# Kernel tuning notes

Measured on AMD Instinct MI355X. Metric: run time of the kernel, lower is better.

The kernel has to match this reference:

```python
import jax, jax.numpy as jnp
import numpy as np

L, H, P, R = 4096, 1024, 512, 16
DT_MIN, DT_MAX = 1e-3, 1e-1

def setup_inputs() -> dict:
    key = jax.random.key(0)
    ks = jax.random.split(key, 16)
    return {
        "input_sequence": jax.random.normal(ks[0], (L, H), jnp.float32),
        # HiPPO-like eigenvalues: negative real part, spread imaginary part
        "Lambda_re": (-0.5 * jax.random.uniform(ks[1], (P,), jnp.float32) - 1e-2),
        "Lambda_im": 3.0 * jax.random.normal(ks[2], (P,), jnp.float32),
        "B_re": jax.random.normal(ks[3], (P, H), jnp.float32) / np.float32(np.sqrt(H)),
        "B_im": jax.random.normal(ks[4], (P, H), jnp.float32) / np.float32(np.sqrt(H)),
        "C_re": jax.random.normal(ks[5], (H, 2 * P), jnp.float32) / np.float32(np.sqrt(2 * P)),
        "C_im": jax.random.normal(ks[6], (H, 2 * P), jnp.float32) / np.float32(np.sqrt(2 * P)),
        "E_re": 0.01 * jax.random.normal(ks[7], (P, R), jnp.float32),
        "E_im": 0.01 * jax.random.normal(ks[8], (P, R), jnp.float32),
        "F_re": 0.01 * jax.random.normal(ks[9], (R, P), jnp.float32),
        "F_im": 0.01 * jax.random.normal(ks[10], (R, P), jnp.float32),
        "D": jax.random.normal(ks[11], (H,), jnp.float32),
        "log_step": np.float32(np.log(DT_MIN)) + jax.random.uniform(ks[12], (P,), jnp.float32) * np.float32(np.log(DT_MAX) - np.log(DT_MIN)),
        "Delta_t_diag": 0.01 * jax.random.normal(ks[13], (L, R), jnp.float32),
    }

def _scan_op(q_i, q_j):
    # diagonal linear recurrence combine: x_j = A_j * x_i + b_j
    A_i, b_i = q_i
    A_j, b_j = q_j
    return (A_j * A_i, A_j * b_i + b_j)

def reference(input_sequence, Lambda_re, Lambda_im, B_re, B_im, C_re, C_im,
              E_re, E_im, F_re, F_im, D, log_step, Delta_t_diag):
    # clip_eigs=True: enforce left-half-plane
    Lam = jnp.clip(Lambda_re, None, -1e-4) + 1j * Lambda_im            # (P,)
    step = jnp.exp(log_step)                                           # (P,)  step_rescale=1.0
    # zoh discretization
    Lambda_bar = jnp.exp(Lam * step)                                   # (P,)
    B_tilde = B_re + 1j * B_im                                         # (P,H)
    B_bar = ((Lambda_bar - 1.0) / Lam)[:, None] * B_tilde              # (P,H)
    # Lambda extension: diag(E @ diag(d_l) @ F)[p] = sum_r E[p,r] d_l[r] F[r,p]
    E = E_re + 1j * E_im                                               # (P,R)
    F = F_re + 1j * F_im                                               # (R,P)
    EF = E.T * F                                                       # (R,P)
    ext = Delta_t_diag.astype(EF.dtype) @ EF                           # (L,P)
    Lambda_elements = Lambda_bar[None, :] + ext                        # (L,P)
    Bu_elements = input_sequence.astype(B_bar.dtype) @ B_bar.T         # (L,P)
    _, xs_f = jax.lax.associative_scan(_scan_op, (Lambda_elements, Bu_elements))
    _, xs_b = jax.lax.associative_scan(_scan_op, (Lambda_elements, Bu_elements), reverse=True)
    xs = jnp.concatenate((xs_f, xs_b), axis=-1)                        # (L,2P) bidirectional
    C_tilde = C_re + 1j * C_im                                         # (H,2P)
    ys = 2.0 * (xs @ C_tilde.T).real                                   # conj_sym=True -> 2*Re
    return ys + D * input_sequence                                     # feedthrough
```

## Files before the change

### kernel.cpp

```cpp
#include <hip/hip_runtime.h>

#define LL 4096
#define HH 1024
#define PP 512
#define RR 16
#define CH 128
#define CL 32

typedef _Float16 f16x8 __attribute__((ext_vector_type(8)));
typedef float f32x4 __attribute__((ext_vector_type(4)));
typedef unsigned short u16;
typedef unsigned int u32;

#define MF16(a, b, c) __builtin_amdgcn_mfma_f32_16x16x32_f16(a, b, c, 0, 0, 0)

__device__ __forceinline__ u16 h16(float x) {
  _Float16 h = (_Float16)x;
  return __builtin_bit_cast(u16, h);
}
__device__ __forceinline__ float f16f(u16 v) {
  return (float)__builtin_bit_cast(_Float16, v);
}

__global__ void precompute_kernel(const float* __restrict__ Lre, const float* __restrict__ Lim,
                                  const float* __restrict__ lst,
                                  const float* __restrict__ Ere, const float* __restrict__ Eim,
                                  const float* __restrict__ Fre, const float* __restrict__ Fim,
                                  float* __restrict__ Lbr, float* __restrict__ Lbi,
                                  float* __restrict__ cfr, float* __restrict__ cfi,
                                  float* __restrict__ EFr, float* __restrict__ EFi)
{
  int p = blockIdx.x * blockDim.x + threadIdx.x;
  if (p >= PP) return;
  float lre = fminf(Lre[p], -1e-4f);
  float lim = Lim[p];
  float st  = expf(lst[p]);
  float er  = expf(lre * st);
  float s, c;
  sincosf(lim * st, &s, &c);
  float lbr = er * c, lbi = er * s;
  Lbr[p] = lbr; Lbi[p] = lbi;
  float den = lre * lre + lim * lim;
  float nr  = lbr - 1.0f;
  cfr[p] = (nr * lre + lbi * lim) / den;
  cfi[p] = (lbi * lre - nr * lim) / den;
  for (int r = 0; r < RR; ++r) {
    float e_r = Ere[p * RR + r], e_i = Eim[p * RR + r];
    float f_r = Fre[r * PP + p], f_i = Fim[r * PP + p];
    EFr[r * PP + p] = e_r * f_r - e_i * f_i;
    EFi[r * PP + p] = e_r * f_i + e_i * f_r;
  }
}

__global__ void bbar_kernel(const float* __restrict__ Bre, const float* __restrict__ Bim,
                            const float* __restrict__ cfr, const float* __restrict__ cfi,
                            u16* __restrict__ B1)
{
  int i = blockIdx.x * blockDim.x + threadIdx.x;
  int base = i * 4;
  if (base >= PP * HH) return;
  int p = base >> 10, col = base & 1023;
  float cr = cfr[p], ci = cfi[p];
  float4 br = *(const float4*)&Bre[base];
  float4 bi = *(const float4*)&Bim[base];
  ushort4 rp, ip;
  rp.x = h16(cr*br.x - ci*bi.x); ip.x = h16(cr*bi.x + ci*br.x);
  rp.y = h16(cr*br.y - ci*bi.y); ip.y = h16(cr*bi.y + ci*br.y);
  rp.z = h16(cr*br.z - ci*bi.z); ip.z = h16(cr*bi.z + ci*br.z);
  rp.w = h16(cr*br.w - ci*bi.w); ip.w = h16(cr*bi.w + ci*br.w);
  *(ushort4*)&B1[(size_t)p * 1024 + col] = rp;
  *(ushort4*)&B1[(size_t)(PP + p) * 1024 + col] = ip;
}

__global__ void prep_c_kernel(const float* __restrict__ Cre, const float* __restrict__ Cim,
                              u32* __restrict__ B2)
{
  int i = blockIdx.x * blockDim.x + threadIdx.x;
  int base = i * 4;
  float4 a = *(const float4*)&Cre[base];
  float4 b = *(const float4*)&Cim[base];
  uint4 o;
  o.x = (u32)h16(a.x) | ((u32)h16(-b.x) << 16);
  o.y = (u32)h16(a.y) | ((u32)h16(-b.y) << 16);
  o.z = (u32)h16(a.z) | ((u32)h16(-b.z) << 16);
  o.w = (u32)h16(a.w) | ((u32)h16(-b.w) << 16);
  *(uint4*)&B2[base] = o;
}

__global__ __launch_bounds__(256) void ext_kernel(
    const float* __restrict__ Dt, const float* __restrict__ EFr, const float* __restrict__ EFi,
    u32* __restrict__ LE)
{
  int gid = blockIdx.x * 256 + threadIdx.x;
  int l  = gid >> 7;
  int pq = (gid & 127) << 2;
  float4 ar = {0.f, 0.f, 0.f, 0.f};
  float4 ai = {0.f, 0.f, 0.f, 0.f};
#pragma unroll
  for (int r = 0; r < RR; ++r) {
    float d = Dt[l * RR + r];
    float4 er = *(const float4*)&EFr[r * PP + pq];
    float4 ei = *(const float4*)&EFi[r * PP + pq];
    ar.x = fmaf(d, er.x, ar.x); ar.y = fmaf(d, er.y, ar.y);
    ar.z = fmaf(d, er.z, ar.z); ar.w = fmaf(d, er.w, ar.w);
    ai.x = fmaf(d, ei.x, ai.x); ai.y = fmaf(d, ei.y, ai.y);
    ai.z = fmaf(d, ei.z, ai.z); ai.w = fmaf(d, ei.w, ai.w);
  }
  uint4 o;
  o.x = (u32)h16(ar.x) | ((u32)h16(ai.x) << 16);
  o.y = (u32)h16(ar.y) | ((u32)h16(ai.y) << 16);
  o.z = (u32)h16(ar.z) | ((u32)h16(ai.z) << 16);
  o.w = (u32)h16(ar.w) | ((u32)h16(ai.w) << 16);
  *(uint4*)&LE[(size_t)l * PP + pq] = o;
}

template<int EPI, bool ACVT>
__global__ __launch_bounds__(256) void gemm_k(
    const void* __restrict__ Asrc, const u16* __restrict__ Bsrc, int Kp,
    float* __restrict__ out, const float* __restrict__ Dv,
    const float* __restrict__ Uep)
{
  __shared__ __align__(16) uint4 lds[2 * 16 * 64];
  int bid = blockIdx.x;
  int n0 = ((bid & 7) * 2 + ((bid >> 3) & 1)) * 64;
  int m0 = (bid >> 4) * 64;
  int t = threadIdx.x, lane = t & 63, w = t >> 6;
  int wr = w >> 1, wc = w & 1;
  int rl = lane & 15, kg = lane >> 4;
  int crow = t >> 2, cch = t & 3;
  int NT = Kp / 64;

  const float* Af = (const float*)Asrc;
  const u16*   Ah = (const u16*)Asrc;

  f32x4 acc[2][2];
  acc[0][0] = acc[0][1] = acc[1][0] = acc[1][1] = (f32x4){0.f, 0.f, 0.f, 0.f};

  struct Frags { uint4 a[2]; uint4 b[2]; };
  auto LOAD = [&](int kt) -> Frags {
    Frags f;
    if constexpr (ACVT) {
      const float* p = Af + (size_t)(m0 + crow) * Kp + kt * 64 + cch * 16;
#pragma unroll
      for (int j = 0; j < 2; ++j) {
        float4 a = *(const float4*)(p + j * 8), b = *(const float4*)(p + j * 8 + 4);
        f16x8 r;
        r[0] = (_Float16)a.x; r[1] = (_Float16)a.y; r[2] = (_Float16)a.z; r[3] = (_Float16)a.w;
        r[4] = (_Float16)b.x; r[5] = (_Float16)b.y; r[6] = (_Float16)b.z; r[7] = (_Float16)b.w;
        f.a[j] = __builtin_bit_cast(uint4, r);
      }
    } else {
      const u16* p = Ah + (size_t)(m0 + crow) * Kp + kt * 64 + cch * 16;
      f.a[0] = *(const uint4*)p;
      f.a[1] = *(const uint4*)(p + 8);
    }
    const u16* q = Bsrc + (size_t)(n0 + crow) * Kp + kt * 64 + cch * 16;
    f.b[0] = *(const uint4*)q;
    f.b[1] = *(const uint4*)(q + 8);
    return f;
  };
  auto WRITE = [&](int buf, const Frags& f) {
#pragma unroll
    for (int j = 0; j < 2; ++j) {
      int kq = cch * 2 + j;
      int c = kq & 3;
      int slot = c * 16 + ((crow & 15) ^ (c * 2));
      int segA = (crow >> 4) * 2 + (kq >> 2);
      lds[buf * 1024 + segA * 64 + slot] = f.a[j];
      lds[buf * 1024 + (8 + segA) * 64 + slot] = f.b[j];
    }
  };

  Frags nxt, far;
  WRITE(0, LOAD(0));
  nxt = LOAD(1);
  __syncthreads();

  for (int kt = 0; kt < NT; ++kt) {
    int c = kt & 1;
    if (kt + 2 < NT) far = LOAD(kt + 2);
    int rslot = kg * 16 + (rl ^ (kg * 2));
    f16x8 af[2][2], bf[2][2];
#pragma unroll
    for (int m = 0; m < 2; ++m)
#pragma unroll
      for (int ks = 0; ks < 2; ++ks) {
        int segA = (wr * 2 + m) * 2 + ks;
        int segB = 8 + (wc * 2 + m) * 2 + ks;
        af[m][ks] = __builtin_bit_cast(f16x8, lds[c * 1024 + segA * 64 + rslot]);
        bf[m][ks] = __builtin_bit_cast(f16x8, lds[c * 1024 + segB * 64 + rslot]);
      }
#pragma unroll
    for (int ks = 0; ks < 2; ++ks)
#pragma unroll
      for (int m = 0; m < 2; ++m)
#pragma unroll
        for (int n = 0; n < 2; ++n)
          acc[m][n] = MF16(af[m][ks], bf[n][ks], acc[m][n]);
    if (kt + 1 < NT) WRITE(c ^ 1, nxt);
    nxt = far;
    __syncthreads();
  }

  float* Stg = (float*)lds;
#pragma unroll
  for (int m = 0; m < 2; ++m)
#pragma unroll
    for (int n = 0; n < 2; ++n)
#pragma unroll
      for (int j = 0; j < 4; ++j)
        Stg[(wr * 32 + m * 16 + kg * 4 + j) * 68 + wc * 32 + n * 16 + rl] = acc[m][n][j];
  __syncthreads();
  int col4 = (t & 15) * 4, prow = t >> 4;
#pragma unroll
  for (int i = 0; i < 4; ++i) {
    int r = prow + 16 * i;
    float4 v = *(const float4*)&Stg[r * 68 + col4];
    size_t ob = (size_t)(m0 + r) * 1024 + n0 + col4;
    if constexpr (EPI == 1) {
      float4 u4 = *(const float4*)&Uep[ob];
      float4 dv = *(const float4*)&Dv[n0 + col4];
      v.x = 2.f * v.x + dv.x * u4.x; v.y = 2.f * v.y + dv.y * u4.y;
      v.z = 2.f * v.z + dv.z * u4.z; v.w = 2.f * v.w + dv.w * u4.w;
    }
    *(float4*)&out[ob] = v;
  }
}

__global__ __launch_bounds__(256) void scan_agg_kernel(
    const float* __restrict__ Lbr, const float* __restrict__ Lbi,
    const u32* __restrict__ LE, const float* __restrict__ P,
    float* __restrict__ aggAr, float* __restrict__ aggAi,
    float* __restrict__ aggBr, float* __restrict__ aggBi)
{
  int tid = blockIdx.x * 256 + threadIdx.x;
  int p   = tid & (PP - 1);
  int c   = (tid >> 9) & (CH - 1);
  int dir = tid >> 16;
  float lbr = Lbr[p], lbi = Lbi[p];
  float Ar = 1.f, Ai = 0.f, br = 0.f, bi = 0.f;
  int base = c * CL;
#pragma unroll
  for (int g = 0; g < CL / 8; ++g) {
    float ar8[8], ai8[8], br8[8], bi8[8];
#pragma unroll
    for (int u = 0; u < 8; ++u) {
      int l = base + g * 8 + u;
      int phys = dir ? (LL - 1 - l) : l;
      u32 v = LE[(size_t)phys * PP + p];
      ar8[u] = lbr + f16f((u16)(v & 0xffff));
      ai8[u] = lbi + f16f((u16)(v >> 16));
      br8[u] = P[(size_t)phys * 1024 + p];
      bi8[u] = P[(size_t)phys * 1024 + PP + p];
    }
#pragma unroll
    for (int u = 0; u < 8; ++u) {
      float nAr = ar8[u] * Ar - ai8[u] * Ai;
      float nAi = ar8[u] * Ai + ai8[u] * Ar;
      float nbr = fmaf(ar8[u], br, fmaf(-ai8[u], bi, br8[u]));
      float nbi = fmaf(ar8[u], bi, fmaf( ai8[u], br, bi8[u]));
      Ar = nAr; Ai = nAi; br = nbr; bi = nbi;
    }
  }
  aggAr[tid] = Ar; aggAi[tid] = Ai; aggBr[tid] = br; aggBi[tid] = bi;
}

__global__ __launch_bounds__(256) void scan_carry_kernel(
    const float* __restrict__ aggAr, const float* __restrict__ aggAi,
    const float* __restrict__ aggBr, const float* __restrict__ aggBi,
    float* __restrict__ carR, float* __restrict__ carI)
{
  int tid = blockIdx.x * 256 + threadIdx.x;
  int p   = tid & (PP - 1);
  int dir = tid >> 9;
  float xr = 0.f, xi = 0.f;
  for (int c = 0; c < CH; ++c) {
    int idx = (dir * CH + c) * PP + p;
    carR[idx] = xr; carI[idx] = xi;
    float ar = aggAr[idx], ai = aggAi[idx];
    float br = aggBr[idx], bi = aggBi[idx];
    float nr = fmaf(ar, xr, fmaf(-ai, xi, br));
    float ni = fmaf(ar, xi, fmaf( ai, xr, bi));
    xr = nr; xi = ni;
  }
}

__global__ __launch_bounds__(256) void scan_apply_kernel(
    const float* __restrict__ Lbr, const float* __restrict__ Lbi,
    const u32* __restrict__ LE, const float* __restrict__ P,
    const float* __restrict__ carR, const float* __restrict__ carI,
    u32* __restrict__ A2)
{
  int tid = blockIdx.x * 256 + threadIdx.x;
  int p   = tid & (PP - 1);
  int c   = (tid >> 9) & (CH - 1);
  int dir = tid >> 16;
  float lbr = Lbr[p], lbi = Lbi[p];
  float xr = carR[tid], xi = carI[tid];
  int base = c * CL;
  int cofs = dir * PP + p;
#pragma unroll
  for (int g = 0; g < CL / 8; ++g) {
    float ar8[8], ai8[8], br8[8], bi8[8];
#pragma unroll
    for (int u = 0; u < 8; ++u) {
      int l = base + g * 8 + u;
      int phys = dir ? (LL - 1 - l) : l;
      u32 v = LE[(size_t)phys * PP + p];
      ar8[u] = lbr + f16f((u16)(v & 0xffff));
      ai8[u] = lbi + f16f((u16)(v >> 16));
      br8[u] = P[(size_t)phys * 1024 + p];
      bi8[u] = P[(size_t)phys * 1024 + PP + p];
    }
#pragma unroll
    for (int u = 0; u < 8; ++u) {
      float nr = fmaf(ar8[u], xr, fmaf(-ai8[u], xi, br8[u]));
      float ni = fmaf(ar8[u], xi, fmaf( ai8[u], xr, bi8[u]));
      xr = nr; xi = ni;
      int l = base + g * 8 + u;
      int phys = dir ? (LL - 1 - l) : l;
      A2[(size_t)phys * 1024 + cofs] = (u32)h16(xr) | ((u32)h16(xi) << 16);
    }
  }
}

extern "C" void kernel_launch(void* const* d_in, const int* in_sizes, int n_in,
                              void* d_out, int out_size, void* d_ws, size_t ws_size,
                              hipStream_t stream)
{
  const float* U   = (const float*)d_in[0];
  const float* Lre = (const float*)d_in[1];
  const float* Lim = (const float*)d_in[2];
  const float* Bre = (const float*)d_in[3];
  const float* Bim = (const float*)d_in[4];
  const float* Cre = (const float*)d_in[5];
  const float* Cim = (const float*)d_in[6];
  const float* Ere = (const float*)d_in[7];
  const float* Eim = (const float*)d_in[8];
  const float* Fre = (const float*)d_in[9];
  const float* Fim = (const float*)d_in[10];
  const float* Dv  = (const float*)d_in[11];
  const float* lst = (const float*)d_in[12];
  const float* Dt  = (const float*)d_in[13];
  float* Y = (float*)d_out;

  char* wsb = (char*)d_ws;
  size_t o = 0;
  auto alloc = [&](size_t bytes) -> char* {
    char* r = wsb + o; o += (bytes + 255) & ~(size_t)255; return r;
  };
  float* Lbr = (float*)alloc(PP * 4);
  float* Lbi = (float*)alloc(PP * 4);
  float* cfr = (float*)alloc(PP * 4);
  float* cfi = (float*)alloc(PP * 4);
  float* EFr = (float*)alloc((size_t)RR * PP * 4);
  float* EFi = (float*)alloc((size_t)RR * PP * 4);
  u16* B1 = (u16*)alloc((size_t)1024 * 1024 * 2);
  u32* B2 = (u32*)alloc((size_t)1024 * 1024 * 4);
  u32* LE = (u32*)alloc((size_t)LL * PP * 4);
  float* P = (float*)alloc((size_t)LL * 1024 * 4);
  u32* A2 = (u32*)alloc((size_t)LL * 1024 * 4);
  const int NAGG = 2 * CH * PP;
  float* aggAr = (float*)alloc((size_t)NAGG * 4);
  float* aggAi = (float*)alloc((size_t)NAGG * 4);
  float* aggBr = (float*)alloc((size_t)NAGG * 4);
  float* aggBi = (float*)alloc((size_t)NAGG * 4);
  float* carR  = (float*)alloc((size_t)NAGG * 4);
  float* carI  = (float*)alloc((size_t)NAGG * 4);

  precompute_kernel<<<2, 256, 0, stream>>>(Lre, Lim, lst, Ere, Eim, Fre, Fim,
                                           Lbr, Lbi, cfr, cfi, EFr, EFi);
  bbar_kernel<<<PP * HH / 4 / 256, 256, 0, stream>>>(Bre, Bim, cfr, cfi, B1);
  prep_c_kernel<<<1024 * 1024 / 4 / 256, 256, 0, stream>>>(Cre, Cim, B2);
  ext_kernel<<<LL * PP / 4 / 256, 256, 0, stream>>>(Dt, EFr, EFi, LE);
  gemm_k<0, true><<<1024, 256, 0, stream>>>(U, B1, 1024, P, nullptr, nullptr);
  scan_agg_kernel<<<2 * CH * PP / 256, 256, 0, stream>>>(Lbr, Lbi, LE, P,
                                                         aggAr, aggAi, aggBr, aggBi);
  scan_carry_kernel<<<4, 256, 0, stream>>>(aggAr, aggAi, aggBr, aggBi, carR, carI);
  scan_apply_kernel<<<2 * CH * PP / 256, 256, 0, stream>>>(Lbr, Lbi, LE, P, carR, carI, A2);
  gemm_k<1, false><<<1024, 256, 0, stream>>>(A2, (const u16*)B2, 2048, Y, Dv, U);
}
```

Baseline: 123.9 us.

## Use direct global-to-LDS loads and 64x128 tiles in GEMMs, pre-convert input to fp16

The GEMM kernel now loads tiles straight from global memory into LDS with global_load_lds instead of staging them through registers, and widens each block's tile from 64x64 to 64x128, so the grid shrinks from 1024 to 512 blocks. The in-GEMM fp32-to-fp16 conversion of the input sequence is dropped; a separate kernel now converts it to fp16 beforehand. The aim is lower register pressure and fewer load instructions, plus more reuse per A tile. The cost is an extra kernel launch and extra memory traffic for the fp16 copy, and the pipeline now issues the next tile only one step ahead.

```diff
diff --git a/kernel.cpp b/kernel.cpp
--- a/kernel.cpp
+++ b/kernel.cpp
@@ -20,6 +20,11 @@
 }
 __device__ __forceinline__ float f16f(u16 v) {
   return (float)__builtin_bit_cast(_Float16, v);
+}
+__device__ __forceinline__ void gld16(const void* g, void* l) {
+  __builtin_amdgcn_global_load_lds(
+      (__attribute__((address_space(1))) void*)g,
+      (__attribute__((address_space(3))) void*)l, 16, 0, 0);
 }
 
 __global__ void precompute_kernel(const float* __restrict__ Lre, const float* __restrict__ Lim,
@@ -87,6 +92,18 @@
   *(uint4*)&B2[base] = o;
 }
 
+__global__ __launch_bounds__(256) void uconv_kernel(const float* __restrict__ U,
+                                                    u16* __restrict__ Uh)
+{
+  int i = (blockIdx.x * 256 + threadIdx.x) * 8;
+  float4 a = *(const float4*)&U[i];
+  float4 b = *(const float4*)&U[i + 4];
+  f16x8 r;
+  r[0] = (_Float16)a.x; r[1] = (_Float16)a.y; r[2] = (_Float16)a.z; r[3] = (_Float16)a.w;
+  r[4] = (_Float16)b.x; r[5] = (_Float16)b.y; r[6] = (_Float16)b.z; r[7] = (_Float16)b.w;
+  *(uint4*)&Uh[i] = __builtin_bit_cast(uint4, r);
+}
+
 __global__ __launch_bounds__(256) void ext_kernel(
     const float* __restrict__ Dt, const float* __restrict__ EFr, const float* __restrict__ EFi,
     u32* __restrict__ LE)
@@ -114,91 +131,73 @@
   *(uint4*)&LE[(size_t)l * PP + pq] = o;
 }
 
-template<int EPI, bool ACVT>
+template<int EPI>
 __global__ __launch_bounds__(256) void gemm_k(
-    const void* __restrict__ Asrc, const u16* __restrict__ Bsrc, int Kp,
+    const u16* __restrict__ Asrc, const u16* __restrict__ Bsrc, int Kp,
     float* __restrict__ out, const float* __restrict__ Dv,
     const float* __restrict__ Uep)
 {
-  __shared__ __align__(16) uint4 lds[2 * 16 * 64];
+  __shared__ __align__(16) uint4 lds[2 * 24 * 64];
   int bid = blockIdx.x;
-  int n0 = ((bid & 7) * 2 + ((bid >> 3) & 1)) * 64;
-  int m0 = (bid >> 4) * 64;
+  int n0 = (bid & 7) * 128;
+  int m0 = (bid >> 3) * 64;
   int t = threadIdx.x, lane = t & 63, w = t >> 6;
   int wr = w >> 1, wc = w & 1;
   int rl = lane & 15, kg = lane >> 4;
-  int crow = t >> 2, cch = t & 3;
   int NT = Kp / 64;
 
-  const float* Af = (const float*)Asrc;
-  const u16*   Ah = (const u16*)Asrc;
-
-  f32x4 acc[2][2];
-  acc[0][0] = acc[0][1] = acc[1][0] = acc[1][1] = (f32x4){0.f, 0.f, 0.f, 0.f};
-
-  struct Frags { uint4 a[2]; uint4 b[2]; };
-  auto LOAD = [&](int kt) -> Frags {
-    Frags f;
-    if constexpr (ACVT) {
-      const float* p = Af + (size_t)(m0 + crow) * Kp + kt * 64 + cch * 16;
-#pragma unroll
-      for (int j = 0; j < 2; ++j) {
-        float4 a = *(const float4*)(p + j * 8), b = *(const float4*)(p + j * 8 + 4);
-        f16x8 r;
-        r[0] = (_Float16)a.x; r[1] = (_Float16)a.y; r[2] = (_Float16)a.z; r[3] = (_Float16)a.w;
-        r[4] = (_Float16)b.x; r[5] = (_Float16)b.y; r[6] = (_Float16)b.z; r[7] = (_Float16)b.w;
-        f.a[j] = __builtin_bit_cast(uint4, r);
-      }
-    } else {
-      const u16* p = Ah + (size_t)(m0 + crow) * Kp + kt * 64 + cch * 16;
-      f.a[0] = *(const uint4*)p;
-      f.a[1] = *(const uint4*)(p + 8);
-    }
-    const u16* q = Bsrc + (size_t)(n0 + crow) * Kp + kt * 64 + cch * 16;
-    f.b[0] = *(const uint4*)q;
-    f.b[1] = *(const uint4*)(q + 8);
-    return f;
+  int rowx = rl ^ (2 * kg);
+  const u16* segsrc[6];
+#pragma unroll
+  for (int i = 0; i < 6; ++i) {
+    int s = w * 6 + i;
+    int isB = (s >= 8);
+    int sl = isB ? (s - 8) : s;
+    int row = (sl >> 1) * 16 + rowx;
+    int kq = (sl & 1) * 4 + kg;
+    segsrc[i] = (isB ? (Bsrc + (size_t)(n0 + row) * Kp)
+                     : (Asrc + (size_t)(m0 + row) * Kp)) + kq * 8;
+  }
+
+  f32x4 acc[2][4];
+#pragma unroll
+  for (int m = 0; m < 2; ++m)
+#pragma unroll
+    for (int n = 0; n < 4; ++n) acc[m][n] = (f32x4){0.f, 0.f, 0.f, 0.f};
+
+  auto ISSUE = [&](int kt, int buf) {
+#pragma unroll
+    for (int i = 0; i < 6; ++i)
+      gld16(segsrc[i] + kt * 64, &lds[(buf * 24 + w * 6 + i) * 64]);
   };
-  auto WRITE = [&](int buf, const Frags& f) {
-#pragma unroll
-    for (int j = 0; j < 2; ++j) {
-      int kq = cch * 2 + j;
-      int c = kq & 3;
-      int slot = c * 16 + ((crow & 15) ^ (c * 2));
-      int segA = (crow >> 4) * 2 + (kq >> 2);
-      lds[buf * 1024 + segA * 64 + slot] = f.a[j];
-      lds[buf * 1024 + (8 + segA) * 64 + slot] = f.b[j];
-    }
-  };
-
-  Frags nxt, far;
-  WRITE(0, LOAD(0));
-  nxt = LOAD(1);
+
+  ISSUE(0, 0);
   __syncthreads();
 
   for (int kt = 0; kt < NT; ++kt) {
     int c = kt & 1;
-    if (kt + 2 < NT) far = LOAD(kt + 2);
+    if (kt + 1 < NT) ISSUE(kt + 1, c ^ 1);
     int rslot = kg * 16 + (rl ^ (kg * 2));
-    f16x8 af[2][2], bf[2][2];
+    f16x8 af[2][2], bf[4][2];
 #pragma unroll
     for (int m = 0; m < 2; ++m)
 #pragma unroll
-      for (int ks = 0; ks < 2; ++ks) {
-        int segA = (wr * 2 + m) * 2 + ks;
-        int segB = 8 + (wc * 2 + m) * 2 + ks;
-        af[m][ks] = __builtin_bit_cast(f16x8, lds[c * 1024 + segA * 64 + rslot]);
-        bf[m][ks] = __builtin_bit_cast(f16x8, lds[c * 1024 + segB * 64 + rslot]);
-      }
+      for (int ks = 0; ks < 2; ++ks)
+        af[m][ks] = __builtin_bit_cast(f16x8,
+            lds[(c * 24 + (wr * 2 + m) * 2 + ks) * 64 + rslot]);
+#pragma unroll
+    for (int n = 0; n < 4; ++n)
+#pragma unroll
+      for (int ks = 0; ks < 2; ++ks)
+        bf[n][ks] = __builtin_bit_cast(f16x8,
+            lds[(c * 24 + 8 + (wc * 4 + n) * 2 + ks) * 64 + rslot]);
 #pragma unroll
     for (int ks = 0; ks < 2; ++ks)
 #pragma unroll
       for (int m = 0; m < 2; ++m)
 #pragma unroll
-        for (int n = 0; n < 2; ++n)
+        for (int n = 0; n < 4; ++n)
           acc[m][n] = MF16(af[m][ks], bf[n][ks], acc[m][n]);
-    if (kt + 1 < NT) WRITE(c ^ 1, nxt);
-    nxt = far;
     __syncthreads();
   }
 
@@ -206,16 +205,16 @@
 #pragma unroll
   for (int m = 0; m < 2; ++m)
 #pragma unroll
-    for (int n = 0; n < 2; ++n)
+    for (int n = 0; n < 4; ++n)
 #pragma unroll
       for (int j = 0; j < 4; ++j)
-        Stg[(wr * 32 + m * 16 + kg * 4 + j) * 68 + wc * 32 + n * 16 + rl] = acc[m][n][j];
+        Stg[(wr * 32 + m * 16 + kg * 4 + j) * 132 + wc * 64 + n * 16 + rl] = acc[m][n][j];
   __syncthreads();
-  int col4 = (t & 15) * 4, prow = t >> 4;
-#pragma unroll
-  for (int i = 0; i < 4; ++i) {
-    int r = prow + 16 * i;
-    float4 v = *(const float4*)&Stg[r * 68 + col4];
+  int col4 = (t & 31) * 4, prow = t >> 5;
+#pragma unroll
+  for (int i = 0; i < 8; ++i) {
+    int r = prow + 8 * i;
+    float4 v = *(const float4*)&Stg[r * 132 + col4];
     size_t ob = (size_t)(m0 + r) * 1024 + n0 + col4;
     if constexpr (EPI == 1) {
       float4 u4 = *(const float4*)&Uep[ob];
@@ -357,6 +356,7 @@
   float* EFi = (float*)alloc((size_t)RR * PP * 4);
   u16* B1 = (u16*)alloc((size_t)1024 * 1024 * 2);
   u32* B2 = (u32*)alloc((size_t)1024 * 1024 * 4);
+  u16* Uh = (u16*)alloc((size_t)LL * HH * 2);
   u32* LE = (u32*)alloc((size_t)LL * PP * 4);
   float* P = (float*)alloc((size_t)LL * 1024 * 4);
   u32* A2 = (u32*)alloc((size_t)LL * 1024 * 4);
@@ -372,11 +372,12 @@
                                            Lbr, Lbi, cfr, cfi, EFr, EFi);
   bbar_kernel<<<PP * HH / 4 / 256, 256, 0, stream>>>(Bre, Bim, cfr, cfi, B1);
   prep_c_kernel<<<1024 * 1024 / 4 / 256, 256, 0, stream>>>(Cre, Cim, B2);
+  uconv_kernel<<<LL * HH / 8 / 256, 256, 0, stream>>>(U, Uh);
   ext_kernel<<<LL * PP / 4 / 256, 256, 0, stream>>>(Dt, EFr, EFi, LE);
-  gemm_k<0, true><<<1024, 256, 0, stream>>>(U, B1, 1024, P, nullptr, nullptr);
+  gemm_k<0><<<512, 256, 0, stream>>>(Uh, B1, 1024, P, nullptr, nullptr);
   scan_agg_kernel<<<2 * CH * PP / 256, 256, 0, stream>>>(Lbr, Lbi, LE, P,
                                                          aggAr, aggAi, aggBr, aggBi);
   scan_carry_kernel<<<4, 256, 0, stream>>>(aggAr, aggAi, aggBr, aggBi, carR, carI);
   scan_apply_kernel<<<2 * CH * PP / 256, 256, 0, stream>>>(Lbr, Lbi, LE, P, carR, carI, A2);
-  gemm_k<1, false><<<1024, 256, 0, stream>>>(A2, (const u16*)B2, 2048, Y, Dv, U);
-}
+  gemm_k<1><<<512, 256, 0, stream>>>((const u16*)A2, (const u16*)B2, 2048, Y, Dv, U);
+}
```

Result: slower. 139.4 us (+12.5%).

## Fuse prep kernels and store interleaved fp16 Bu output for scans

Applied to the files above, without the earlier changes.

Merges the B-bar, C-packing and Lambda-extension prep kernels into one launch with block-range dispatch. Reorders B1 rows so the first GEMM yields interleaved real/imag columns, and its epilogue writes packed fp16 pairs instead of fp32, halving the Bu intermediate read twice by the scan kernels. Scans now load one u32 per element instead of two floats from distant columns. Adds fp16 rounding of Bu before the recurrence, a possible accuracy loss.

```diff
diff --git a/kernel.cpp b/kernel.cpp
--- a/kernel.cpp
+++ b/kernel.cpp
@@ -52,72 +52,67 @@
   }
 }
 
-__global__ void bbar_kernel(const float* __restrict__ Bre, const float* __restrict__ Bim,
-                            const float* __restrict__ cfr, const float* __restrict__ cfi,
-                            u16* __restrict__ B1)
-{
-  int i = blockIdx.x * blockDim.x + threadIdx.x;
-  int base = i * 4;
-  if (base >= PP * HH) return;
-  int p = base >> 10, col = base & 1023;
-  float cr = cfr[p], ci = cfi[p];
-  float4 br = *(const float4*)&Bre[base];
-  float4 bi = *(const float4*)&Bim[base];
-  ushort4 rp, ip;
-  rp.x = h16(cr*br.x - ci*bi.x); ip.x = h16(cr*bi.x + ci*br.x);
-  rp.y = h16(cr*br.y - ci*bi.y); ip.y = h16(cr*bi.y + ci*br.y);
-  rp.z = h16(cr*br.z - ci*bi.z); ip.z = h16(cr*bi.z + ci*br.z);
-  rp.w = h16(cr*br.w - ci*bi.w); ip.w = h16(cr*bi.w + ci*br.w);
-  *(ushort4*)&B1[(size_t)p * 1024 + col] = rp;
-  *(ushort4*)&B1[(size_t)(PP + p) * 1024 + col] = ip;
-}
-
-__global__ void prep_c_kernel(const float* __restrict__ Cre, const float* __restrict__ Cim,
-                              u32* __restrict__ B2)
-{
-  int i = blockIdx.x * blockDim.x + threadIdx.x;
-  int base = i * 4;
-  float4 a = *(const float4*)&Cre[base];
-  float4 b = *(const float4*)&Cim[base];
-  uint4 o;
-  o.x = (u32)h16(a.x) | ((u32)h16(-b.x) << 16);
-  o.y = (u32)h16(a.y) | ((u32)h16(-b.y) << 16);
-  o.z = (u32)h16(a.z) | ((u32)h16(-b.z) << 16);
-  o.w = (u32)h16(a.w) | ((u32)h16(-b.w) << 16);
-  *(uint4*)&B2[base] = o;
-}
-
-__global__ __launch_bounds__(256) void ext_kernel(
-    const float* __restrict__ Dt, const float* __restrict__ EFr, const float* __restrict__ EFi,
-    u32* __restrict__ LE)
-{
-  int gid = blockIdx.x * 256 + threadIdx.x;
-  int l  = gid >> 7;
-  int pq = (gid & 127) << 2;
-  float4 ar = {0.f, 0.f, 0.f, 0.f};
-  float4 ai = {0.f, 0.f, 0.f, 0.f};
-#pragma unroll
-  for (int r = 0; r < RR; ++r) {
-    float d = Dt[l * RR + r];
-    float4 er = *(const float4*)&EFr[r * PP + pq];
-    float4 ei = *(const float4*)&EFi[r * PP + pq];
-    ar.x = fmaf(d, er.x, ar.x); ar.y = fmaf(d, er.y, ar.y);
-    ar.z = fmaf(d, er.z, ar.z); ar.w = fmaf(d, er.w, ar.w);
-    ai.x = fmaf(d, ei.x, ai.x); ai.y = fmaf(d, ei.y, ai.y);
-    ai.z = fmaf(d, ei.z, ai.z); ai.w = fmaf(d, ei.w, ai.w);
-  }
-  uint4 o;
-  o.x = (u32)h16(ar.x) | ((u32)h16(ai.x) << 16);
-  o.y = (u32)h16(ar.y) | ((u32)h16(ai.y) << 16);
-  o.z = (u32)h16(ar.z) | ((u32)h16(ai.z) << 16);
-  o.w = (u32)h16(ar.w) | ((u32)h16(ai.w) << 16);
-  *(uint4*)&LE[(size_t)l * PP + pq] = o;
+__global__ __launch_bounds__(256) void prep2_kernel(
+    const float* __restrict__ Bre, const float* __restrict__ Bim,
+    const float* __restrict__ cfr, const float* __restrict__ cfi,
+    const float* __restrict__ Cre, const float* __restrict__ Cim,
+    const float* __restrict__ Dt, const float* __restrict__ EFr,
+    const float* __restrict__ EFi,
+    u16* __restrict__ B1, u32* __restrict__ B2, u32* __restrict__ LE)
+{
+  int g = blockIdx.x, t = threadIdx.x;
+  if (g < 512) {
+    int base = (g * 256 + t) * 4;
+    int p = base >> 10, col = base & 1023;
+    float cr = cfr[p], ci = cfi[p];
+    float4 br = *(const float4*)&Bre[base];
+    float4 bi = *(const float4*)&Bim[base];
+    ushort4 rp, ip;
+    rp.x = h16(cr*br.x - ci*bi.x); ip.x = h16(cr*bi.x + ci*br.x);
+    rp.y = h16(cr*br.y - ci*bi.y); ip.y = h16(cr*bi.y + ci*br.y);
+    rp.z = h16(cr*br.z - ci*bi.z); ip.z = h16(cr*bi.z + ci*br.z);
+    rp.w = h16(cr*br.w - ci*bi.w); ip.w = h16(cr*bi.w + ci*br.w);
+    *(ushort4*)&B1[(size_t)(2 * p) * 1024 + col] = rp;
+    *(ushort4*)&B1[(size_t)(2 * p + 1) * 1024 + col] = ip;
+  } else if (g < 1536) {
+    int base = ((g - 512) * 256 + t) * 4;
+    float4 a = *(const float4*)&Cre[base];
+    float4 b = *(const float4*)&Cim[base];
+    uint4 o;
+    o.x = (u32)h16(a.x) | ((u32)h16(-b.x) << 16);
+    o.y = (u32)h16(a.y) | ((u32)h16(-b.y) << 16);
+    o.z = (u32)h16(a.z) | ((u32)h16(-b.z) << 16);
+    o.w = (u32)h16(a.w) | ((u32)h16(-b.w) << 16);
+    *(uint4*)&B2[base] = o;
+  } else {
+    int gid = (g - 1536) * 256 + t;
+    int l  = gid >> 7;
+    int pq = (gid & 127) << 2;
+    float4 ar = {0.f, 0.f, 0.f, 0.f};
+    float4 ai = {0.f, 0.f, 0.f, 0.f};
+#pragma unroll
+    for (int r = 0; r < RR; ++r) {
+      float d = Dt[l * RR + r];
+      float4 er = *(const float4*)&EFr[r * PP + pq];
+      float4 ei = *(const float4*)&EFi[r * PP + pq];
+      ar.x = fmaf(d, er.x, ar.x); ar.y = fmaf(d, er.y, ar.y);
+      ar.z = fmaf(d, er.z, ar.z); ar.w = fmaf(d, er.w, ar.w);
+      ai.x = fmaf(d, ei.x, ai.x); ai.y = fmaf(d, ei.y, ai.y);
+      ai.z = fmaf(d, ei.z, ai.z); ai.w = fmaf(d, ei.w, ai.w);
+    }
+    uint4 o;
+    o.x = (u32)h16(ar.x) | ((u32)h16(ai.x) << 16);
+    o.y = (u32)h16(ar.y) | ((u32)h16(ai.y) << 16);
+    o.z = (u32)h16(ar.z) | ((u32)h16(ai.z) << 16);
+    o.w = (u32)h16(ar.w) | ((u32)h16(ai.w) << 16);
+    *(uint4*)&LE[(size_t)l * PP + pq] = o;
+  }
 }
 
 template<int EPI, bool ACVT>
 __global__ __launch_bounds__(256) void gemm_k(
     const void* __restrict__ Asrc, const u16* __restrict__ Bsrc, int Kp,
-    float* __restrict__ out, const float* __restrict__ Dv,
+    void* __restrict__ outv, const float* __restrict__ Dv,
     const float* __restrict__ Uep)
 {
   __shared__ __align__(16) uint4 lds[2 * 16 * 64];
@@ -216,20 +211,29 @@
   for (int i = 0; i < 4; ++i) {
     int r = prow + 16 * i;
     float4 v = *(const float4*)&Stg[r * 68 + col4];
-    size_t ob = (size_t)(m0 + r) * 1024 + n0 + col4;
-    if constexpr (EPI == 1) {
-      float4 u4 = *(const float4*)&Uep[ob];
-      float4 dv = *(const float4*)&Dv[n0 + col4];
-      v.x = 2.f * v.x + dv.x * u4.x; v.y = 2.f * v.y + dv.y * u4.y;
-      v.z = 2.f * v.z + dv.z * u4.z; v.w = 2.f * v.w + dv.w * u4.w;
-    }
-    *(float4*)&out[ob] = v;
+    if constexpr (EPI == 2) {
+      uint2 pk;
+      pk.x = (u32)h16(v.x) | ((u32)h16(v.y) << 16);
+      pk.y = (u32)h16(v.z) | ((u32)h16(v.w) << 16);
+      u32* outp = (u32*)outv;
+      *(uint2*)&outp[(size_t)(m0 + r) * 512 + (n0 + col4) / 2] = pk;
+    } else {
+      float* out = (float*)outv;
+      size_t ob = (size_t)(m0 + r) * 1024 + n0 + col4;
+      if constexpr (EPI == 1) {
+        float4 u4 = *(const float4*)&Uep[ob];
+        float4 dv = *(const float4*)&Dv[n0 + col4];
+        v.x = 2.f * v.x + dv.x * u4.x; v.y = 2.f * v.y + dv.y * u4.y;
+        v.z = 2.f * v.z + dv.z * u4.z; v.w = 2.f * v.w + dv.w * u4.w;
+      }
+      *(float4*)&out[ob] = v;
+    }
   }
 }
 
 __global__ __launch_bounds__(256) void scan_agg_kernel(
     const float* __restrict__ Lbr, const float* __restrict__ Lbi,
-    const u32* __restrict__ LE, const float* __restrict__ P,
+    const u32* __restrict__ LE, const u32* __restrict__ P2,
     float* __restrict__ aggAr, float* __restrict__ aggAi,
     float* __restrict__ aggBr, float* __restrict__ aggBi)
 {
@@ -248,10 +252,11 @@
       int l = base + g * 8 + u;
       int phys = dir ? (LL - 1 - l) : l;
       u32 v = LE[(size_t)phys * PP + p];
+      u32 bv = P2[(size_t)phys * PP + p];
       ar8[u] = lbr + f16f((u16)(v & 0xffff));
       ai8[u] = lbi + f16f((u16)(v >> 16));
-      br8[u] = P[(size_t)phys * 1024 + p];
-      bi8[u] = P[(size_t)phys * 1024 + PP + p];
+      br8[u] = f16f((u16)(bv & 0xffff));
+      bi8[u] = f16f((u16)(bv >> 16));
     }
 #pragma unroll
     for (int u = 0; u < 8; ++u) {
@@ -287,7 +292,7 @@
 
 __global__ __launch_bounds__(256) void scan_apply_kernel(
     const float* __restrict__ Lbr, const float* __restrict__ Lbi,
-    const u32* __restrict__ LE, const float* __restrict__ P,
+    const u32* __restrict__ LE, const u32* __restrict__ P2,
     const float* __restrict__ carR, const float* __restrict__ carI,
     u32* __restrict__ A2)
 {
@@ -307,10 +312,11 @@
       int l = base + g * 8 + u;
       int phys = dir ? (LL - 1 - l) : l;
       u32 v = LE[(size_t)phys * PP + p];
+      u32 bv = P2[(size_t)phys * PP + p];
       ar8[u] = lbr + f16f((u16)(v & 0xffff));
       ai8[u] = lbi + f16f((u16)(v >> 16));
-      br8[u] = P[(size_t)phys * 1024 + p];
-      bi8[u] = P[(size_t)phys * 1024 + PP + p];
+      br8[u] = f16f((u16)(bv & 0xffff));
+      bi8[u] = f16f((u16)(bv >> 16));
     }
 #pragma unroll
     for (int u = 0; u < 8; ++u) {
@@ -358,7 +364,7 @@
   u16* B1 = (u16*)alloc((size_t)1024 * 1024 * 2);
   u32* B2 = (u32*)alloc((size_t)1024 * 1024 * 4);
   u32* LE = (u32*)alloc((size_t)LL * PP * 4);
-  float* P = (float*)alloc((size_t)LL * 1024 * 4);
+  u32* P2 = (u32*)alloc((size_t)LL * PP * 4);
   u32* A2 = (u32*)alloc((size_t)LL * 1024 * 4);
   const int NAGG = 2 * CH * PP;
   float* aggAr = (float*)alloc((size_t)NAGG * 4);
@@ -370,13 +376,12 @@
 
   precompute_kernel<<<2, 256, 0, stream>>>(Lre, Lim, lst, Ere, Eim, Fre, Fim,
                                            Lbr, Lbi, cfr, cfi, EFr, EFi);
-  bbar_kernel<<<PP * HH / 4 / 256, 256, 0, stream>>>(Bre, Bim, cfr, cfi, B1);
-  prep_c_kernel<<<1024 * 1024 / 4 / 256, 256, 0, stream>>>(Cre, Cim, B2);
-  ext_kernel<<<LL * PP / 4 / 256, 256, 0, stream>>>(Dt, EFr, EFi, LE);
-  gemm_k<0, true><<<1024, 256, 0, stream>>>(U, B1, 1024, P, nullptr, nullptr);
-  scan_agg_kernel<<<2 * CH * PP / 256, 256, 0, stream>>>(Lbr, Lbi, LE, P,
+  prep2_kernel<<<3584, 256, 0, stream>>>(Bre, Bim, cfr, cfi, Cre, Cim,
+                                         Dt, EFr, EFi, B1, B2, LE);
+  gemm_k<2, true><<<1024, 256, 0, stream>>>(U, B1, 1024, P2, nullptr, nullptr);
+  scan_agg_kernel<<<2 * CH * PP / 256, 256, 0, stream>>>(Lbr, Lbi, LE, P2,
                                                          aggAr, aggAi, aggBr, aggBi);
   scan_carry_kernel<<<4, 256, 0, stream>>>(aggAr, aggAi, aggBr, aggBi, carR, carI);
-  scan_apply_kernel<<<2 * CH * PP / 256, 256, 0, stream>>>(Lbr, Lbi, LE, P, carR, carI, A2);
+  scan_apply_kernel<<<2 * CH * PP / 256, 256, 0, stream>>>(Lbr, Lbi, LE, P2, carR, carI, A2);
   gemm_k<1, false><<<1024, 256, 0, stream>>>(A2, (const u16*)B2, 2048, Y, Dv, U);
 }
```

Measured after the change: 114.5 us. -7.6%, faster.
